# Kernel tuning notes

Measured on AMD Instinct MI355X. Metric: run time of the kernel, lower is better.

## Reference

```python
import jax, jax.numpy as jnp
import numpy as np
import math

B, T, C, H = 4, 1024, 1024, 16
R = 32.0
MAX_SPAN = 1024  # block_size
SPAN_REG = 2e-06


def setup_inputs() -> dict:
    key = jax.random.key(0)
    k1, k2, k3 = jax.random.split(key, 3)
    x = jax.random.normal(k1, (B, T, C), dtype=jnp.float32)
    Wqkv = jax.random.normal(k2, (C, 3 * C), dtype=jnp.float32) * 0.02
    Wproj = jax.random.normal(k3, (C, C), dtype=jnp.float32) * 0.02
    span_params = jnp.zeros((H,), dtype=jnp.float32)
    stride_params = jnp.zeros((H, 2), dtype=jnp.float32)
    return {"x": x, "Wqkv": Wqkv, "Wproj": Wproj,
            "span_params": span_params, "stride_params": stride_params}


def reference(x, Wqkv, Wproj, span_params, stride_params):
    b, t, c = x.shape
    h = span_params.shape[0]
    hd = c // h

    qkv = x @ Wqkv                                  # [B,T,3C]
    q, k, v = jnp.split(qkv, 3, axis=-1)
    q = q.reshape(b, t, h, hd).transpose(0, 2, 1, 3)  # [B,H,T,hd]
    k = k.reshape(b, t, h, hd).transpose(0, 2, 1, 3)
    v = v.reshape(b, t, h, hd).transpose(0, 2, 1, 3)

    att = jnp.einsum('bhqd,bhkd->bhqk', q, k) * (1.0 / math.sqrt(hd))

    i = jnp.arange(t)[:, None]
    j = jnp.arange(t)[None, :]
    rel = (i - j).astype(jnp.float32)               # relative position i-j
    causal = i >= j                                 # stride-1 pattern == tril
    allowed2 = (i == j) | ((i > j) & ((i - j) % 2 == 0))  # stride-2 pattern

    spans = jax.nn.sigmoid(span_params) * MAX_SPAN  # [H]
    sw = jax.nn.softmax(stride_params, axis=-1)     # [H,2]

    sp = spans[:, None, None]                       # [H,1,1]
    # soft ramp mask: 1 inside span, linear falloff over R, 0 outside / disallowed
    m1 = jnp.where(causal,  jnp.clip((R + sp - rel) / R, 0.0, 1.0), 0.0)  # [H,T,T]
    m2 = jnp.where(allowed2, jnp.clip((R + sp - rel) / R, 0.0, 1.0), 0.0)
    mask = sw[:, 0, None, None] * m1 + sw[:, 1, None, None] * m2          # [H,T,T]

    # unnormalized exp weighting (no max-subtraction), causal -inf fill
    wexp = jnp.exp(jnp.where(causal, att, -jnp.inf)) * mask               # [B,H,T,T]
    att_n = wexp / jnp.sum(wexp, axis=-1, keepdims=True)

    y = jnp.einsum('bhqk,bhkd->bhqd', att_n, v)
    y = y.transpose(0, 2, 1, 3).reshape(b, t, c)
    y = y @ Wproj

    span_loss = SPAN_REG * jnp.sum(spans) / h
    return y, span_loss
```

## Files before the change

kernel.cpp:

```cpp
#include <hip/hip_runtime.h>
#include <math.h>

#define BATCH 4
#define SEQ   1024
#define CH    1024
#define NH    16
#define HD    64
#define N3    3072

typedef unsigned short u16;
typedef unsigned int   u32;
typedef __attribute__((ext_vector_type(8))) __bf16 bf16x8;
typedef __attribute__((ext_vector_type(4))) float  f32x4;
typedef __attribute__((ext_vector_type(4))) u32    u32x4;

__device__ __forceinline__ u32 f2bf(float f) {
    u32 x = __float_as_uint(f);
    return (x + 0x7fffu + ((x >> 16) & 1u)) >> 16;
}

__device__ __forceinline__ void gload_lds16(const u16* g, u16* l) {
    __builtin_amdgcn_global_load_lds(
        (const __attribute__((address_space(1))) void*)g,
        (__attribute__((address_space(3))) void*)l, 16, 0, 0);
}

__global__ __launch_bounds__(256) void conv_bf16_kernel(
    const float* __restrict__ in, u16* __restrict__ out, int n)
{
    int i = (blockIdx.x * 256 + threadIdx.x) * 8;
    if (i >= n) return;
    float4 a = *(const float4*)&in[i];
    float4 b = *(const float4*)&in[i + 4];
    int4 p;
    p.x = (int)(f2bf(a.x) | (f2bf(a.y) << 16));
    p.y = (int)(f2bf(a.z) | (f2bf(a.w) << 16));
    p.z = (int)(f2bf(b.x) | (f2bf(b.y) << 16));
    p.w = (int)(f2bf(b.z) | (f2bf(b.w) << 16));
    *(int4*)&out[i] = p;
}

__global__ __launch_bounds__(256) void transpose_both_kernel(
    const float* __restrict__ Wqkv, const float* __restrict__ Wproj,
    u16* __restrict__ wqT, u16* __restrict__ wpT)
{
    __shared__ float tile[32][33];
    int bx = blockIdx.x;
    const float* W;
    u16* WT;
    int N;
    if (bx < N3 / 32) { W = Wqkv; WT = wqT; N = N3; }
    else              { bx -= N3 / 32; W = Wproj; WT = wpT; N = CH; }
    const int n0 = bx * 32, k0 = blockIdx.y * 32;
    const int tx = threadIdx.x & 31, ty = threadIdx.x >> 5;
    #pragma unroll
    for (int p = 0; p < 4; p++)
        tile[ty + p * 8][tx] = W[(size_t)(k0 + ty + p * 8) * N + n0 + tx];
    __syncthreads();
    #pragma unroll
    for (int p = 0; p < 4; p++)
        WT[(size_t)(n0 + ty + p * 8) * CH + k0 + tx] = (u16)f2bf(tile[tx][ty + p * 8]);
}

__global__ __launch_bounds__(256) void gemm_qkv_mfma(
    const u16* __restrict__ A, const u16* __restrict__ BT,
    u16* __restrict__ qb, u16* __restrict__ kbuf, u16* __restrict__ vtb)
{
    __shared__ __align__(16) u16 As[128 * 32];
    __shared__ __align__(16) u16 Bs[128 * 32];

    const int tid = threadIdx.x;
    const int lane = tid & 63;
    const int w = tid >> 6;
    const int wr = w >> 1, wc = w & 1;
    const int m0 = blockIdx.y * 128, n0 = blockIdx.x * 128;

    const int srow = lane >> 2;
    const int sk   = (lane & 3) * 8;
    const u16* gA0 = A  + (size_t)(m0 + w * 16 + srow) * CH + sk;
    const u16* gA1 = A  + (size_t)(m0 + (w + 4) * 16 + srow) * CH + sk;
    const u16* gB0 = BT + (size_t)(n0 + w * 16 + srow) * CH + sk;
    const u16* gB1 = BT + (size_t)(n0 + (w + 4) * 16 + srow) * CH + sk;
    u16* lA0 = As + w * 16 * 32;
    u16* lA1 = As + (w + 4) * 16 * 32;
    u16* lB0 = Bs + w * 16 * 32;
    u16* lB1 = Bs + (w + 4) * 16 * 32;

    const int ln = lane & 15, quad = lane >> 4;
    const int afo = (wr * 64 + ln) * 32 + quad * 8;
    const int bfo = (wc * 64 + ln) * 32 + quad * 8;

    f32x4 acc[4][4];
    #pragma unroll
    for (int i = 0; i < 4; i++)
        #pragma unroll
        for (int j = 0; j < 4; j++) acc[i][j] = (f32x4)(0.f);

    for (int k0 = 0; k0 < CH; k0 += 32) {
        __syncthreads();
        gload_lds16(gA0 + k0, lA0);
        gload_lds16(gA1 + k0, lA1);
        gload_lds16(gB0 + k0, lB0);
        gload_lds16(gB1 + k0, lB1);
        __syncthreads();
        bf16x8 af[4], bfr[4];
        #pragma unroll
        for (int mi = 0; mi < 4; mi++) af[mi]  = *(const bf16x8*)&As[afo + mi * 512];
        #pragma unroll
        for (int ni = 0; ni < 4; ni++) bfr[ni] = *(const bf16x8*)&Bs[bfo + ni * 512];
        #pragma unroll
        for (int mi = 0; mi < 4; mi++)
            #pragma unroll
            for (int ni = 0; ni < 4; ni++)
                acc[mi][ni] = __builtin_amdgcn_mfma_f32_16x16x32_bf16(
                    af[mi], bfr[ni], acc[mi][ni], 0, 0, 0);
    }

    const int which = (n0 >> 10);
    if (which == 2) {
        #pragma unroll
        for (int ni = 0; ni < 4; ni++) {
            const int n = n0 + wc * 64 + ni * 16 + ln;
            const int h = (n >> 6) & 15;
            const int d = n & 63;
            #pragma unroll
            for (int mi = 0; mi < 4; mi++) {
                const int m = m0 + wr * 64 + mi * 16 + quad * 4;
                const int b = m >> 10, t = m & 1023;
                int2 pv;
                pv.x = (int)(f2bf(acc[mi][ni][0]) | (f2bf(acc[mi][ni][1]) << 16));
                pv.y = (int)(f2bf(acc[mi][ni][2]) | (f2bf(acc[mi][ni][3]) << 16));
                *(int2*)&vtb[(((size_t)(b * NH + h)) * HD + d) * SEQ + t] = pv;
            }
        }
    } else {
        u16* dst = (which == 0) ? qb : kbuf;
        #pragma unroll
        for (int ni = 0; ni < 4; ni++) {
            const int n = n0 + wc * 64 + ni * 16 + ln;
            const int h = (n >> 6) & 15;
            const int d = n & 63;
            #pragma unroll
            for (int mi = 0; mi < 4; mi++) {
                #pragma unroll
                for (int r = 0; r < 4; r++) {
                    const int m = m0 + wr * 64 + mi * 16 + quad * 4 + r;
                    const int b = m >> 10, t = m & 1023;
                    dst[(((size_t)(b * NH + h)) * SEQ + t) * HD + d] =
                        (u16)f2bf(acc[mi][ni][r]);
                }
            }
        }
    }
}

__global__ __launch_bounds__(256) void gemm_proj_mfma(
    const u16* __restrict__ A, const u16* __restrict__ BT, float* __restrict__ out,
    const float* __restrict__ sp, float* __restrict__ loss_out)
{
    __shared__ __align__(16) u16 As[64 * 32];
    __shared__ __align__(16) u16 Bs[128 * 32];

    const int tid = threadIdx.x;
    const int lane = tid & 63;
    const int w = tid >> 6;
    const int wr = w >> 1, wc = w & 1;
    const int m0 = blockIdx.y * 64, n0 = blockIdx.x * 128;

    if (blockIdx.x == 0 && blockIdx.y == 0 && tid == 0) {
        float s = 0.f;
        #pragma unroll
        for (int h = 0; h < NH; h++) {
            float sig = 1.f / (1.f + __expf(-sp[h]));
            s += sig * 1024.f;
        }
        loss_out[0] = 2e-6f * s / (float)NH;
    }

    const int srow = lane >> 2;
    const int sk   = (lane & 3) * 8;
    const u16* gA0 = A  + (size_t)(m0 + w * 16 + srow) * CH + sk;
    const u16* gB0 = BT + (size_t)(n0 + w * 16 + srow) * CH + sk;
    const u16* gB1 = BT + (size_t)(n0 + (w + 4) * 16 + srow) * CH + sk;
    u16* lA0 = As + w * 16 * 32;
    u16* lB0 = Bs + w * 16 * 32;
    u16* lB1 = Bs + (w + 4) * 16 * 32;

    const int ln = lane & 15, quad = lane >> 4;
    const int afo = (wr * 32 + ln) * 32 + quad * 8;
    const int bfo = (wc * 64 + ln) * 32 + quad * 8;

    f32x4 acc[2][4];
    #pragma unroll
    for (int i = 0; i < 2; i++)
        #pragma unroll
        for (int j = 0; j < 4; j++) acc[i][j] = (f32x4)(0.f);

    for (int k0 = 0; k0 < CH; k0 += 32) {
        __syncthreads();
        gload_lds16(gA0 + k0, lA0);
        gload_lds16(gB0 + k0, lB0);
        gload_lds16(gB1 + k0, lB1);
        __syncthreads();
        bf16x8 af[2], bfr[4];
        #pragma unroll
        for (int mi = 0; mi < 2; mi++) af[mi]  = *(const bf16x8*)&As[afo + mi * 512];
        #pragma unroll
        for (int ni = 0; ni < 4; ni++) bfr[ni] = *(const bf16x8*)&Bs[bfo + ni * 512];
        #pragma unroll
        for (int mi = 0; mi < 2; mi++)
            #pragma unroll
            for (int ni = 0; ni < 4; ni++)
                acc[mi][ni] = __builtin_amdgcn_mfma_f32_16x16x32_bf16(
                    af[mi], bfr[ni], acc[mi][ni], 0, 0, 0);
    }

    #pragma unroll
    for (int ni = 0; ni < 4; ni++) {
        const int n = n0 + wc * 64 + ni * 16 + ln;
        #pragma unroll
        for (int mi = 0; mi < 2; mi++) {
            #pragma unroll
            for (int r = 0; r < 4; r++) {
                const int m = m0 + wr * 32 + mi * 16 + quad * 4 + r;
                out[(size_t)m * CH + n] = acc[mi][ni][r];
            }
        }
    }
}

__global__ __launch_bounds__(256) void attn_mfma_kernel(
    const u16* __restrict__ qg, const u16* __restrict__ kg,
    const u16* __restrict__ vt,
    const float* __restrict__ span_params, const float* __restrict__ stride_params,
    u16* __restrict__ yb)
{
    __shared__ __align__(16) u16 Ks[64 * 64];
    __shared__ __align__(16) u16 Vs[64 * 64];
    __shared__ __align__(16) u16 Ps[4][16 * 64];

    const int tid  = threadIdx.x;
    const int lane = tid & 63;
    const int w    = tid >> 6;
    const int ln   = lane & 15, quad = lane >> 4;
    const int lm7  = ln & 7;

    const int blk = blockIdx.x;
    const int bh  = blk & 63;
    const int it  = 15 - (blk >> 6);
    const int h   = bh & (NH - 1);
    const int b   = bh >> 4;
    const int it0 = it << 6;
    const int row_base = it0 + (w << 4);

    const float span  = 1024.f / (1.f + __expf(-span_params[h]));
    const float limit = 32.f + span;
    const float e0 = __expf(stride_params[2 * h + 0]);
    const float e1 = __expf(stride_params[2 * h + 1]);
    const float swO = e0 / (e0 + e1);
    const float c1 = limit * (1.f / 32.f);

    const size_t hb  = (size_t)bh * SEQ;
    const size_t hvt = (size_t)bh * HD;

    const u16* qp = qg + (hb + row_base + ln) * HD + quad * 8;
    bf16x8 aq0 = *(const bf16x8*)qp;
    bf16x8 aq1 = *(const bf16x8*)(qp + 32);

    u32x4 onesw; onesw.x = onesw.y = onesw.z = onesw.w = 0x3f803f80u;
    const bf16x8 onesf = __builtin_bit_cast(bf16x8, onesw);

    f32x4 acc_o[4];
    #pragma unroll
    for (int di = 0; di < 4; di++) acc_o[di] = (f32x4)(0.f);
    f32x4 acc_s = (f32x4)(0.f);

    int jmin = it0 - (int)limit - 1;
    if (jmin < 0) jmin = 0;
    const int jt0 = jmin & ~63;

    const int srow = lane >> 3;
    const int schk = lane & 7;
    const int cs   = schk ^ srow;
    const int ra   = w * 8 + srow;
    const u16* pk0 = kg + (hb + ra) * HD + cs * 8;
    const u16* pk1 = pk0 + 32 * HD;
    const u16* pv0 = vt + (hvt + ra) * SEQ + cs * 8;
    const u16* pv1 = pv0 + 32 * SEQ;
    u16* Ksw0 = Ks + w * 512;
    u16* Ksw1 = Ks + 2048 + w * 512;
    u16* Vsw0 = Vs + w * 512;
    u16* Vsw1 = Vs + 2048 + w * 512;

    u16* Psw = Ps[w];

    for (int jt = jt0; jt <= it0; jt += 64) {
        __syncthreads();
        gload_lds16(pk0 + (size_t)jt * HD, Ksw0);
        gload_lds16(pk1 + (size_t)jt * HD, Ksw1);
        gload_lds16(pv0 + jt, Vsw0);
        gload_lds16(pv1 + jt, Vsw1);
        __syncthreads();

        bool sk[4];
        #pragma unroll
        for (int ni = 0; ni < 4; ni++) {
            const int col0 = jt + ni * 16;
            sk[ni] = (row_base + 15 < col0) ||
                     ((float)(row_base - (col0 + 15)) >= limit);
        }
        const bool nz0 = !sk[0] || !sk[1];
        const bool nz1 = !sk[2] || !sk[3];

        #pragma unroll
        for (int ni = 0; ni < 4; ni++) {
            const int col0 = jt + ni * 16;
            const int cbase = ni * 2 + (ln >> 3);
            if (sk[ni]) {
                if ((ni < 2) ? nz0 : nz1) {
                    #pragma unroll
                    for (int r = 0; r < 4; r++) {
                        const int il = quad * 4 + r;
                        Psw[il * 64 + (cbase ^ (il & 7)) * 8 + lm7] = 0;
                    }
                }
                continue;
            }
            const int krow = ni * 16 + ln;
            bf16x8 bk0 = *(const bf16x8*)&Ks[krow * 64 + ((quad ^ lm7) * 8)];
            bf16x8 bk1 = *(const bf16x8*)&Ks[krow * 64 + (((quad + 4) ^ lm7) * 8)];
            f32x4 s = __builtin_amdgcn_mfma_f32_16x16x32_bf16(aq0, bk0, (f32x4)(0.f), 0, 0, 0);
            s = __builtin_amdgcn_mfma_f32_16x16x32_bf16(aq1, bk1, s, 0, 0, 0);
            #pragma unroll
            for (int r = 0; r < 4; r++) {
                const int il  = quad * 4 + r;
                const int rel = (row_base + il) - (col0 + ln);
                float clip = fminf(fmaxf(fmaf((float)rel, -(1.f / 32.f), c1), 0.f), 1.f);
                float fac  = (rel & 1) ? swO : 1.0f;
                float wt   = (rel < 0) ? 0.f : clip * fac;
                float wv   = __expf(s[r] * 0.125f) * wt;
                Psw[il * 64 + (cbase ^ (il & 7)) * 8 + lm7] = (u16)f2bf(wv);
            }
        }

        if (nz0) {
            bf16x8 ap0 = *(const bf16x8*)&Psw[ln * 64 + (quad ^ lm7) * 8];
            acc_s = __builtin_amdgcn_mfma_f32_16x16x32_bf16(ap0, onesf, acc_s, 0, 0, 0);
            #pragma unroll
            for (int di = 0; di < 4; di++) {
                const int vrow = di * 16 + ln;
                bf16x8 bv0 = *(const bf16x8*)&Vs[vrow * 64 + ((quad ^ lm7) * 8)];
                acc_o[di] = __builtin_amdgcn_mfma_f32_16x16x32_bf16(ap0, bv0, acc_o[di], 0, 0, 0);
            }
        }
        if (nz1) {
            bf16x8 ap1 = *(const bf16x8*)&Psw[ln * 64 + ((quad + 4) ^ lm7) * 8];
            acc_s = __builtin_amdgcn_mfma_f32_16x16x32_bf16(ap1, onesf, acc_s, 0, 0, 0);
            #pragma unroll
            for (int di = 0; di < 4; di++) {
                const int vrow = di * 16 + ln;
                bf16x8 bv1 = *(const bf16x8*)&Vs[vrow * 64 + (((quad + 4) ^ lm7) * 8)];
                acc_o[di] = __builtin_amdgcn_mfma_f32_16x16x32_bf16(ap1, bv1, acc_o[di], 0, 0, 0);
            }
        }
    }

    #pragma unroll
    for (int r = 0; r < 4; r++) {
        const int t = row_base + quad * 4 + r;
        const float inv = 1.f / acc_s[r];
        const size_t rowoff = ((size_t)(b * SEQ + t)) * CH + h * HD;
        #pragma unroll
        for (int di = 0; di < 4; di++)
            yb[rowoff + di * 16 + ln] = (u16)f2bf(acc_o[di][r] * inv);
    }
}

extern "C" void kernel_launch(void* const* d_in, const int* in_sizes, int n_in,
                              void* d_out, int out_size, void* d_ws, size_t ws_size,
                              hipStream_t stream)
{
    const float* x            = (const float*)d_in[0];
    const float* Wqkv         = (const float*)d_in[1];
    const float* Wproj        = (const float*)d_in[2];
    const float* span_params  = (const float*)d_in[3];
    const float* stride_param = (const float*)d_in[4];
    float* out = (float*)d_out;

    const size_t SZ = (size_t)BATCH * NH * SEQ * HD;
    u16* base = (u16*)d_ws;
    u16* qb  = base;
    u16* kb  = qb + SZ;
    u16* vtb = kb + SZ;
    u16* yb  = vtb + SZ;
    u16* xb  = yb + SZ;
    u16* wqT = xb + SZ;
    u16* wpT = wqT + (size_t)CH * N3;

    conv_bf16_kernel<<<dim3((int)(SZ / (256 * 8))), 256, 0, stream>>>(x, xb, (int)SZ);
    transpose_both_kernel<<<dim3((N3 + CH) / 32, CH / 32), 256, 0, stream>>>(
        Wqkv, Wproj, wqT, wpT);

    gemm_qkv_mfma<<<dim3(N3 / 128, (BATCH * SEQ) / 128), 256, 0, stream>>>(
        xb, wqT, qb, kb, vtb);

    attn_mfma_kernel<<<dim3(BATCH * NH * (SEQ / 64)), 256, 0, stream>>>(
        qb, kb, vtb, span_params, stride_param, yb);

    gemm_proj_mfma<<<dim3(CH / 128, (BATCH * SEQ) / 64), 256, 0, stream>>>(
        yb, wpT, out, span_params, out + SZ);
}
```

Measured before the change: 164.7 us.

## Double-buffer attention K/V tiles, process 128 query rows per block, fuse prep kernels

The attention kernel now handles two 64-row query subtiles per block, so each K/V tile loaded into LDS is reused by twice as many rows. K/V loads are double-buffered: the next tile is issued before computing on the current one, which removes one barrier per iteration. The x conversion and weight transposes are merged into one prep launch. The price is half as many attention blocks (512), more registers and LDS per block, and possible load imbalance on the causal triangle.

```diff
diff --git a/kernel.cpp b/kernel.cpp
--- a/kernel.cpp
+++ b/kernel.cpp
@@ -25,33 +25,34 @@
         (__attribute__((address_space(3))) void*)l, 16, 0, 0);
 }
 
-__global__ __launch_bounds__(256) void conv_bf16_kernel(
-    const float* __restrict__ in, u16* __restrict__ out, int n)
-{
-    int i = (blockIdx.x * 256 + threadIdx.x) * 8;
-    if (i >= n) return;
-    float4 a = *(const float4*)&in[i];
-    float4 b = *(const float4*)&in[i + 4];
-    int4 p;
-    p.x = (int)(f2bf(a.x) | (f2bf(a.y) << 16));
-    p.y = (int)(f2bf(a.z) | (f2bf(a.w) << 16));
-    p.z = (int)(f2bf(b.x) | (f2bf(b.y) << 16));
-    p.w = (int)(f2bf(b.z) | (f2bf(b.w) << 16));
-    *(int4*)&out[i] = p;
-}
-
-__global__ __launch_bounds__(256) void transpose_both_kernel(
-    const float* __restrict__ Wqkv, const float* __restrict__ Wproj,
-    u16* __restrict__ wqT, u16* __restrict__ wpT)
+__global__ __launch_bounds__(256) void prep_kernel(
+    const float* __restrict__ x, const float* __restrict__ Wqkv,
+    const float* __restrict__ Wproj,
+    u16* __restrict__ xb, u16* __restrict__ wqT, u16* __restrict__ wpT)
 {
     __shared__ float tile[32][33];
-    int bx = blockIdx.x;
+    const int blk = blockIdx.x;
+    if (blk < 2048) {
+        int i = (blk * 256 + threadIdx.x) * 8;
+        float4 a = *(const float4*)&x[i];
+        float4 b = *(const float4*)&x[i + 4];
+        int4 p;
+        p.x = (int)(f2bf(a.x) | (f2bf(a.y) << 16));
+        p.y = (int)(f2bf(a.z) | (f2bf(a.w) << 16));
+        p.z = (int)(f2bf(b.x) | (f2bf(b.y) << 16));
+        p.w = (int)(f2bf(b.z) | (f2bf(b.w) << 16));
+        *(int4*)&xb[i] = p;
+        return;
+    }
+    const int bx2 = blk - 2048;
+    int nt = bx2 & 127;
+    const int kt = bx2 >> 7;
     const float* W;
     u16* WT;
     int N;
-    if (bx < N3 / 32) { W = Wqkv; WT = wqT; N = N3; }
-    else              { bx -= N3 / 32; W = Wproj; WT = wpT; N = CH; }
-    const int n0 = bx * 32, k0 = blockIdx.y * 32;
+    if (nt < 96) { W = Wqkv; WT = wqT; N = N3; }
+    else         { nt -= 96; W = Wproj; WT = wpT; N = CH; }
+    const int n0 = nt * 32, k0 = kt * 32;
     const int tx = threadIdx.x & 31, ty = threadIdx.x >> 5;
     #pragma unroll
     for (int p = 0; p < 4; p++)
@@ -235,9 +236,9 @@
     const float* __restrict__ span_params, const float* __restrict__ stride_params,
     u16* __restrict__ yb)
 {
-    __shared__ __align__(16) u16 Ks[64 * 64];
-    __shared__ __align__(16) u16 Vs[64 * 64];
-    __shared__ __align__(16) u16 Ps[4][16 * 64];
+    __shared__ __align__(16) u16 Ks[2][64 * 64];
+    __shared__ __align__(16) u16 Vs[2][64 * 64];
+    __shared__ __align__(16) u16 Ps[4][2][16 * 64];
 
     const int tid  = threadIdx.x;
     const int lane = tid & 63;
@@ -247,11 +248,10 @@
 
     const int blk = blockIdx.x;
     const int bh  = blk & 63;
-    const int it  = 15 - (blk >> 6);
+    const int itile = 7 - (blk >> 6);
     const int h   = bh & (NH - 1);
     const int b   = bh >> 4;
-    const int it0 = it << 6;
-    const int row_base = it0 + (w << 4);
+    const int it0 = itile << 7;
 
     const float span  = 1024.f / (1.f + __expf(-span_params[h]));
     const float limit = 32.f + span;
@@ -263,21 +263,30 @@
     const size_t hb  = (size_t)bh * SEQ;
     const size_t hvt = (size_t)bh * HD;
 
-    const u16* qp = qg + (hb + row_base + ln) * HD + quad * 8;
-    bf16x8 aq0 = *(const bf16x8*)qp;
-    bf16x8 aq1 = *(const bf16x8*)(qp + 32);
+    const int rb0 = it0 + (w << 4);
+    const int rb1 = rb0 + 64;
+    const u16* qp0 = qg + (hb + rb0 + ln) * HD + quad * 8;
+    const u16* qp1 = qg + (hb + rb1 + ln) * HD + quad * 8;
+    bf16x8 aqA[2], aqB[2];
+    aqA[0] = *(const bf16x8*)qp0;  aqB[0] = *(const bf16x8*)(qp0 + 32);
+    aqA[1] = *(const bf16x8*)qp1;  aqB[1] = *(const bf16x8*)(qp1 + 32);
 
     u32x4 onesw; onesw.x = onesw.y = onesw.z = onesw.w = 0x3f803f80u;
     const bf16x8 onesf = __builtin_bit_cast(bf16x8, onesw);
 
-    f32x4 acc_o[4];
-    #pragma unroll
-    for (int di = 0; di < 4; di++) acc_o[di] = (f32x4)(0.f);
-    f32x4 acc_s = (f32x4)(0.f);
+    f32x4 acc_o[2][4];
+    f32x4 acc_s[2];
+    #pragma unroll
+    for (int p = 0; p < 2; p++) {
+        acc_s[p] = (f32x4)(0.f);
+        #pragma unroll
+        for (int di = 0; di < 4; di++) acc_o[p][di] = (f32x4)(0.f);
+    }
 
     int jmin = it0 - (int)limit - 1;
     if (jmin < 0) jmin = 0;
     const int jt0 = jmin & ~63;
+    const int last = it0 + 64;
 
     const int srow = lane >> 3;
     const int schk = lane & 7;
@@ -287,92 +296,110 @@
     const u16* pk1 = pk0 + 32 * HD;
     const u16* pv0 = vt + (hvt + ra) * SEQ + cs * 8;
     const u16* pv1 = pv0 + 32 * SEQ;
-    u16* Ksw0 = Ks + w * 512;
-    u16* Ksw1 = Ks + 2048 + w * 512;
-    u16* Vsw0 = Vs + w * 512;
-    u16* Vsw1 = Vs + 2048 + w * 512;
-
-    u16* Psw = Ps[w];
-
-    for (int jt = jt0; jt <= it0; jt += 64) {
+
+    gload_lds16(pk0 + (size_t)jt0 * HD, &Ks[0][w * 512]);
+    gload_lds16(pk1 + (size_t)jt0 * HD, &Ks[0][2048 + w * 512]);
+    gload_lds16(pv0 + jt0,              &Vs[0][w * 512]);
+    gload_lds16(pv1 + jt0,              &Vs[0][2048 + w * 512]);
+
+    int cur = 0;
+    for (int jt = jt0; jt <= last; jt += 64, cur ^= 1) {
         __syncthreads();
-        gload_lds16(pk0 + (size_t)jt * HD, Ksw0);
-        gload_lds16(pk1 + (size_t)jt * HD, Ksw1);
-        gload_lds16(pv0 + jt, Vsw0);
-        gload_lds16(pv1 + jt, Vsw1);
-        __syncthreads();
-
-        bool sk[4];
-        #pragma unroll
-        for (int ni = 0; ni < 4; ni++) {
-            const int col0 = jt + ni * 16;
-            sk[ni] = (row_base + 15 < col0) ||
-                     ((float)(row_base - (col0 + 15)) >= limit);
-        }
-        const bool nz0 = !sk[0] || !sk[1];
-        const bool nz1 = !sk[2] || !sk[3];
-
-        #pragma unroll
-        for (int ni = 0; ni < 4; ni++) {
-            const int col0 = jt + ni * 16;
-            const int cbase = ni * 2 + (ln >> 3);
-            if (sk[ni]) {
-                if ((ni < 2) ? nz0 : nz1) {
-                    #pragma unroll
-                    for (int r = 0; r < 4; r++) {
-                        const int il = quad * 4 + r;
-                        Psw[il * 64 + (cbase ^ (il & 7)) * 8 + lm7] = 0;
+
+        const int nxt = jt + 64;
+        if (nxt <= last) {
+            gload_lds16(pk0 + (size_t)nxt * HD, &Ks[cur ^ 1][w * 512]);
+            gload_lds16(pk1 + (size_t)nxt * HD, &Ks[cur ^ 1][2048 + w * 512]);
+            gload_lds16(pv0 + nxt,              &Vs[cur ^ 1][w * 512]);
+            gload_lds16(pv1 + nxt,              &Vs[cur ^ 1][2048 + w * 512]);
+        }
+
+        const u16* Kc = Ks[cur];
+        const u16* Vc = Vs[cur];
+
+        #pragma unroll
+        for (int p = 0; p < 2; p++) {
+            const int row_base = (p == 0) ? rb0 : rb1;
+            bool sk[4];
+            #pragma unroll
+            for (int ni = 0; ni < 4; ni++) {
+                const int col0 = jt + ni * 16;
+                sk[ni] = (row_base + 15 < col0) ||
+                         ((float)(row_base - (col0 + 15)) >= limit);
+            }
+            const bool nz0 = !sk[0] || !sk[1];
+            const bool nz1 = !sk[2] || !sk[3];
+            if (!nz0 && !nz1) continue;
+
+            u16* Psw = &Ps[w][p][0];
+            const bf16x8 qa = aqA[p], qb_ = aqB[p];
+
+            #pragma unroll
+            for (int ni = 0; ni < 4; ni++) {
+                const int col0 = jt + ni * 16;
+                const int cbase = ni * 2 + (ln >> 3);
+                if (sk[ni]) {
+                    if ((ni < 2) ? nz0 : nz1) {
+                        #pragma unroll
+                        for (int r = 0; r < 4; r++) {
+                            const int il = quad * 4 + r;
+                            Psw[il * 64 + (cbase ^ (il & 7)) * 8 + lm7] = 0;
+                        }
                     }
+                    continue;
                 }
-                continue;
-            }
-            const int krow = ni * 16 + ln;
-            bf16x8 bk0 = *(const bf16x8*)&Ks[krow * 64 + ((quad ^ lm7) * 8)];
-            bf16x8 bk1 = *(const bf16x8*)&Ks[krow * 64 + (((quad + 4) ^ lm7) * 8)];
-            f32x4 s = __builtin_amdgcn_mfma_f32_16x16x32_bf16(aq0, bk0, (f32x4)(0.f), 0, 0, 0);
-            s = __builtin_amdgcn_mfma_f32_16x16x32_bf16(aq1, bk1, s, 0, 0, 0);
-            #pragma unroll
-            for (int r = 0; r < 4; r++) {
-                const int il  = quad * 4 + r;
-                const int rel = (row_base + il) - (col0 + ln);
-                float clip = fminf(fmaxf(fmaf((float)rel, -(1.f / 32.f), c1), 0.f), 1.f);
-                float fac  = (rel & 1) ? swO : 1.0f;
-                float wt   = (rel < 0) ? 0.f : clip * fac;
-                float wv   = __expf(s[r] * 0.125f) * wt;
-                Psw[il * 64 + (cbase ^ (il & 7)) * 8 + lm7] = (u16)f2bf(wv);
-            }
-        }
-
-        if (nz0) {
-            bf16x8 ap0 = *(const bf16x8*)&Psw[ln * 64 + (quad ^ lm7) * 8];
-            acc_s = __builtin_amdgcn_mfma_f32_16x16x32_bf16(ap0, onesf, acc_s, 0, 0, 0);
-            #pragma unroll
-            for (int di = 0; di < 4; di++) {
-                const int vrow = di * 16 + ln;
-                bf16x8 bv0 = *(const bf16x8*)&Vs[vrow * 64 + ((quad ^ lm7) * 8)];
-                acc_o[di] = __builtin_amdgcn_mfma_f32_16x16x32_bf16(ap0, bv0, acc_o[di], 0, 0, 0);
-            }
-        }
-        if (nz1) {
-            bf16x8 ap1 = *(const bf16x8*)&Psw[ln * 64 + ((quad + 4) ^ lm7) * 8];
-            acc_s = __builtin_amdgcn_mfma_f32_16x16x32_bf16(ap1, onesf, acc_s, 0, 0, 0);
-            #pragma unroll
-            for (int di = 0; di < 4; di++) {
-                const int vrow = di * 16 + ln;
-                bf16x8 bv1 = *(const bf16x8*)&Vs[vrow * 64 + (((quad + 4) ^ lm7) * 8)];
-                acc_o[di] = __builtin_amdgcn_mfma_f32_16x16x32_bf16(ap1, bv1, acc_o[di], 0, 0, 0);
-            }
-        }
-    }
-
-    #pragma unroll
-    for (int r = 0; r < 4; r++) {
-        const int t = row_base + quad * 4 + r;
-        const float inv = 1.f / acc_s[r];
-        const size_t rowoff = ((size_t)(b * SEQ + t)) * CH + h * HD;
-        #pragma unroll
-        for (int di = 0; di < 4; di++)
-            yb[rowoff + di * 16 + ln] = (u16)f2bf(acc_o[di][r] * inv);
+                const int krow = ni * 16 + ln;
+                bf16x8 bk0 = *(const bf16x8*)&Kc[krow * 64 + ((quad ^ lm7) * 8)];
+                bf16x8 bk1 = *(const bf16x8*)&Kc[krow * 64 + (((quad + 4) ^ lm7) * 8)];
+                f32x4 s = __builtin_amdgcn_mfma_f32_16x16x32_bf16(qa, bk0, (f32x4)(0.f), 0, 0, 0);
+                s = __builtin_amdgcn_mfma_f32_16x16x32_bf16(qb_, bk1, s, 0, 0, 0);
+                #pragma unroll
+                for (int r = 0; r < 4; r++) {
+                    const int il  = quad * 4 + r;
+                    const int rel = (row_base + il) - (col0 + ln);
+                    float clip = fminf(fmaxf(fmaf((float)rel, -(1.f / 32.f), c1), 0.f), 1.f);
+                    float fac  = (rel & 1) ? swO : 1.0f;
+                    float wt   = (rel < 0) ? 0.f : clip * fac;
+                    float wv   = __expf(s[r] * 0.125f) * wt;
+                    Psw[il * 64 + (cbase ^ (il & 7)) * 8 + lm7] = (u16)f2bf(wv);
+                }
+            }
+
+            if (nz0) {
+                bf16x8 ap0 = *(const bf16x8*)&Psw[ln * 64 + (quad ^ lm7) * 8];
+                acc_s[p] = __builtin_amdgcn_mfma_f32_16x16x32_bf16(ap0, onesf, acc_s[p], 0, 0, 0);
+                #pragma unroll
+                for (int di = 0; di < 4; di++) {
+                    const int vrow = di * 16 + ln;
+                    bf16x8 bv0 = *(const bf16x8*)&Vc[vrow * 64 + ((quad ^ lm7) * 8)];
+                    acc_o[p][di] = __builtin_amdgcn_mfma_f32_16x16x32_bf16(ap0, bv0, acc_o[p][di], 0, 0, 0);
+                }
+            }
+            if (nz1) {
+                bf16x8 ap1 = *(const bf16x8*)&Psw[ln * 64 + ((quad + 4) ^ lm7) * 8];
+                acc_s[p] = __builtin_amdgcn_mfma_f32_16x16x32_bf16(ap1, onesf, acc_s[p], 0, 0, 0);
+                #pragma unroll
+                for (int di = 0; di < 4; di++) {
+                    const int vrow = di * 16 + ln;
+                    bf16x8 bv1 = *(const bf16x8*)&Vc[vrow * 64 + (((quad + 4) ^ lm7) * 8)];
+                    acc_o[p][di] = __builtin_amdgcn_mfma_f32_16x16x32_bf16(ap1, bv1, acc_o[p][di], 0, 0, 0);
+                }
+            }
+        }
+    }
+
+    #pragma unroll
+    for (int p = 0; p < 2; p++) {
+        const int row_base = (p == 0) ? rb0 : rb1;
+        #pragma unroll
+        for (int r = 0; r < 4; r++) {
+            const int t = row_base + quad * 4 + r;
+            const float inv = 1.f / acc_s[p][r];
+            const size_t rowoff = ((size_t)(b * SEQ + t)) * CH + h * HD;
+            #pragma unroll
+            for (int di = 0; di < 4; di++)
+                yb[rowoff + di * 16 + ln] = (u16)f2bf(acc_o[p][di][r] * inv);
+        }
     }
 }
 
@@ -397,14 +424,12 @@
     u16* wqT = xb + SZ;
     u16* wpT = wqT + (size_t)CH * N3;
 
-    conv_bf16_kernel<<<dim3((int)(SZ / (256 * 8))), 256, 0, stream>>>(x, xb, (int)SZ);
-    transpose_both_kernel<<<dim3((N3 + CH) / 32, CH / 32), 256, 0, stream>>>(
-        Wqkv, Wproj, wqT, wpT);
+    prep_kernel<<<dim3(6144), 256, 0, stream>>>(x, Wqkv, Wproj, xb, wqT, wpT);
 
     gemm_qkv_mfma<<<dim3(N3 / 128, (BATCH * SEQ) / 128), 256, 0, stream>>>(
         xb, wqT, qb, kb, vtb);
 
-    attn_mfma_kernel<<<dim3(BATCH * NH * (SEQ / 64)), 256, 0, stream>>>(
+    attn_mfma_kernel<<<dim3(BATCH * NH * (SEQ / 128)), 256, 0, stream>>>(
         qb, kb, vtb, span_params, stride_param, yb);
 
     gemm_proj_mfma<<<dim3(CH / 128, (BATCH * SEQ) / 64), 256, 0, stream>>>(
```

New measurement: 169.0 us. +2.7%, slower.
